# Kernel optimization log

Hardware: AMD Instinct MI355X
Metric: run time of the kernel (lower is better)

## Reference

```python
import jax, jax.numpy as jnp
import numpy as np

D_MODEL = 1024
N_HEADS = 16
D_K = D_MODEL // N_HEADS
ROPE_BASE = 10000.0


def _rope_cos_sin(seq_len, dim):
    # matches calc_rope_theta: freqs over even indices of head dim
    freqs = jnp.arange(0, dim, 2, dtype=jnp.float32) / dim
    inv_freq = 1.0 / (ROPE_BASE ** freqs)                      # [dim/2]
    pos = jnp.arange(seq_len, dtype=jnp.float32)               # [S]
    ang = pos[:, None] * inv_freq[None, :]                     # [S, dim/2]
    return jnp.cos(ang), jnp.sin(ang)


def _apply_rope(x, cos, sin):
    # x: [N, S, dk]; complex pairs are consecutive elements (view_as_complex)
    x0 = x[..., 0::2]
    x1 = x[..., 1::2]
    r = x0 * cos - x1 * sin
    i = x0 * sin + x1 * cos
    return jnp.stack([r, i], axis=-1).reshape(x.shape)


def setup_inputs() -> dict:
    key = jax.random.key(0)
    ks = jax.random.split(key, 11)
    B, S, D = 4, 1024, D_MODEL
    w = lambda k: jax.random.normal(k, (D, D), dtype=jnp.float32) * 0.02
    b = lambda k: jax.random.normal(k, (D,), dtype=jnp.float32) * 0.02
    return {
        "q": jax.random.normal(ks[0], (B, S, D), dtype=jnp.float32),
        "k": jax.random.normal(ks[1], (B, S, D), dtype=jnp.float32),
        "v": jax.random.normal(ks[2], (B, S, D), dtype=jnp.float32),
        "Wq": w(ks[3]), "bq": b(ks[4]),
        "Wk": w(ks[5]), "bk": b(ks[6]),
        "Wv": w(ks[7]), "bv": b(ks[8]),
        "Wo": w(ks[9]), "bo": b(ks[10]),
    }


def reference(q, k, v, Wq, bq, Wk, bk, Wv, bv, Wo, bo):
    B, S, D = q.shape
    H, dk = N_HEADS, D_K
    qp = (q @ Wq + bq).reshape(B, S, H, dk)
    kp = (k @ Wk + bk).reshape(B, S, H, dk)
    vp = (v @ Wv + bv).reshape(B, S, H, dk)

    cos, sin = _rope_cos_sin(S, dk)
    # Faithful to source: raw reshape (B,S,H,dk)->(-1,S,dk) before RoPE
    qp = _apply_rope(qp.reshape(-1, S, dk), cos, sin).reshape(B, S, H, dk)
    kp = _apply_rope(kp.reshape(-1, S, dk), cos, sin).reshape(B, S, H, dk)

    qh = qp.transpose(0, 2, 1, 3)  # [B,H,S,dk]
    kh = kp.transpose(0, 2, 1, 3)
    vh = vp.transpose(0, 2, 1, 3)

    scores = jnp.einsum("bhqd,bhkd->bhqk", qh, kh) / jnp.sqrt(jnp.float32(dk))
    attn = jax.nn.softmax(scores, axis=-1)
    out = jnp.einsum("bhqk,bhkd->bhqd", attn, vh)
    out = out.transpose(0, 2, 1, 3).reshape(B, S, D)
    return out @ Wo + bo
```

## Files before the change

### kernel.cpp

```cpp
#include <hip/hip_runtime.h>

typedef __attribute__((ext_vector_type(8))) short bf16x8;
typedef __attribute__((ext_vector_type(4))) short short4v;
typedef __attribute__((ext_vector_type(4))) float f32x4;
typedef __attribute__((ext_vector_type(2))) unsigned u32x2;

#define MFMA16x16x32(a, b, c) __builtin_amdgcn_mfma_f32_16x16x32_bf16((a), (b), (c), 0, 0, 0)

__device__ __forceinline__ short f2bf(float f) {
    unsigned u = __builtin_bit_cast(unsigned, f);
    u += 0x7FFFu + ((u >> 16) & 1u);
    return (short)(u >> 16);
}

__device__ __forceinline__ unsigned cvtpk(float lo, float hi) {
    unsigned r;
    asm("v_cvt_pk_bf16_f32 %0, %1, %2" : "=v"(r) : "v"(lo), "v"(hi));
    return r;
}

__device__ __forceinline__ void gl_lds16(const void* g, void* l) {
    __builtin_amdgcn_global_load_lds((__attribute__((address_space(1))) void*)g,
                                     (__attribute__((address_space(3))) void*)l,
                                     16, 0, 0);
}

__device__ __forceinline__ void cvt16(const float* __restrict__ p, bf16x8& lo, bf16x8& hi) {
    f32x4 a = *(const f32x4*)(p);
    f32x4 b = *(const f32x4*)(p + 4);
    f32x4 c = *(const f32x4*)(p + 8);
    f32x4 d = *(const f32x4*)(p + 12);
#pragma unroll
    for (int i = 0; i < 4; ++i) {
        lo[i]     = f2bf(a[i]);
        lo[i + 4] = f2bf(b[i]);
        hi[i]     = f2bf(c[i]);
        hi[i + 4] = f2bf(d[i]);
    }
}

__global__ __launch_bounds__(256) void prep(const float* __restrict__ q,
                                            const float* __restrict__ k,
                                            const float* __restrict__ v,
                                            const float* __restrict__ w0,
                                            const float* __restrict__ w1,
                                            const float* __restrict__ w2,
                                            const float* __restrict__ w3,
                                            short* __restrict__ y,
                                            short* __restrict__ wt) {
    __shared__ short t[64][80];
    int bid = blockIdx.x, tid = threadIdx.x;
    if (bid < 3072) {
        int sel = bid >> 10;
        const float* x = sel == 0 ? q : (sel == 1 ? k : v);
        short* yy = y + (size_t)sel * (1 << 22);
        int i = ((bid & 1023) * 256 + tid) * 16;
        bf16x8 lo, hi;
        cvt16(x + i, lo, hi);
        *(bf16x8*)(yy + i)     = lo;
        *(bf16x8*)(yy + i + 8) = hi;
        return;
    }
    int tz = bid - 3072;
    int z = tz >> 8, rem = tz & 255, bx = rem & 15, by = rem >> 4;
    const float* W = z == 0 ? w0 : (z == 1 ? w1 : (z == 2 ? w2 : w3));
    short* Wt = wt + (size_t)z * (1 << 20);
    int sr = tid >> 2, sc = (tid & 3) * 16;
    bf16x8 lo, hi;
    cvt16(W + (by * 64 + sr) * 1024 + bx * 64 + sc, lo, hi);
    *(bf16x8*)&t[sr][sc]     = lo;
    *(bf16x8*)&t[sr][sc + 8] = hi;
    __syncthreads();
    bf16x8 o0, o1;
#pragma unroll
    for (int i = 0; i < 8; ++i) {
        o0[i] = t[sc + i][sr];
        o1[i] = t[sc + 8 + i][sr];
    }
    short* dst = Wt + (bx * 64 + sr) * 1024 + by * 64 + sc;
    *(bf16x8*)(dst)     = o0;
    *(bf16x8*)(dst + 8) = o1;
}

__global__ __launch_bounds__(512) void gemm_qkv(const short* __restrict__ A0,
                                                const short* __restrict__ A1,
                                                const short* __restrict__ A2,
                                                const short* __restrict__ wt,
                                                const float* __restrict__ b0,
                                                const float* __restrict__ b1,
                                                const float* __restrict__ b2,
                                                short* __restrict__ d0,
                                                short* __restrict__ d1,
                                                short* __restrict__ d2,
                                                int zoff) {
    __shared__ short As[3][128 * 64];
    __shared__ short Bs[3][128 * 64];
    const int K = 1024;
    int flat = blockIdx.x;
    int xcd = flat & 7, j = flat >> 3;
    int bm = xcd * 4 + (j & 3);
    int bn = (j >> 2) & 7;
    int z  = zoff + (j >> 5);
    const short* A    = z == 0 ? A0 : (z == 1 ? A1 : A2);
    const short* Bt   = wt + (size_t)z * (1 << 20);
    const float* bias = z == 0 ? b0 : (z == 1 ? b1 : b2);
    short* dst        = z == 0 ? d0 : (z == 1 ? d1 : d2);

    int tid = threadIdx.x;
    int wave = tid >> 6, lane = tid & 63;
    int quad = lane >> 4, l16 = lane & 15;
    int wm = (wave >> 2) * 64, wn = (wave & 3) * 32;
    int swr = l16 & 7;

    f32x4 acc[4][2] = {};

    auto stage = [&](int b, int t) {
        int kb = t * 64;
#pragma unroll
        for (int jj = 0; jj < 2; ++jj) {
            int c = jj * 512 + tid;
            int row = c >> 3, sl = c & 7;
            gl_lds16(A + (bm * 128 + row) * K + kb + ((sl ^ (row & 7)) * 8),
                     &As[b][c * 8]);
        }
#pragma unroll
        for (int jj = 0; jj < 2; ++jj) {
            int c = jj * 512 + tid;
            int row = c >> 3, sl = c & 7;
            gl_lds16(Bt + (bn * 128 + row) * K + kb + ((sl ^ (row & 7)) * 8),
                     &Bs[b][c * 8]);
        }
    };

    stage(0, 0);
    stage(1, 1);

    int cur = 0;
    for (int t = 0; t < 16; ++t) {
        asm volatile("s_waitcnt vmcnt(4)" ::: "memory");
        __builtin_amdgcn_sched_barrier(0);
        __builtin_amdgcn_s_barrier();
        __builtin_amdgcn_sched_barrier(0);
        int pre = cur >= 1 ? cur - 1 : 2;
        stage(pre, (t + 2) & 15);
#pragma unroll
        for (int ks = 0; ks < 2; ++ks) {
            bf16x8 bf[2], af[4];
#pragma unroll
            for (int ni = 0; ni < 2; ++ni)
                bf[ni] = *(const bf16x8*)
                    &Bs[cur][(wn + ni * 16 + l16) * 64 + (((ks * 4 + quad) ^ swr) * 8)];
#pragma unroll
            for (int mi = 0; mi < 4; ++mi)
                af[mi] = *(const bf16x8*)
                    &As[cur][(wm + mi * 16 + l16) * 64 + (((ks * 4 + quad) ^ swr) * 8)];
            __builtin_amdgcn_s_setprio(1);
#pragma unroll
            for (int mi = 0; mi < 4; ++mi)
#pragma unroll
                for (int ni = 0; ni < 2; ++ni)
                    acc[mi][ni] = MFMA16x16x32(af[mi], bf[ni], acc[mi][ni]);
            __builtin_amdgcn_s_setprio(0);
        }
        cur = cur < 2 ? cur + 1 : 0;
    }

    int row0 = bm * 128 + wm;
    int col0 = bn * 128 + wn;
#pragma unroll
    for (int mi = 0; mi < 4; ++mi) {
#pragma unroll
        for (int ni = 0; ni < 2; ++ni) {
            int gn = col0 + ni * 16 + l16;
            float bv = bias[gn];
            f32x4 c = acc[mi][ni];
            int h = gn >> 6, dd = gn & 63;
            if (z < 2) {
                float inv = exp2f(-(float)(dd >> 1) * 0.41524101186092029f);
#pragma unroll
                for (int r = 0; r < 4; ++r) {
                    int gm = row0 + mi * 16 + quad * 4 + r;
                    int s = gm & 1023, b = gm >> 10;
                    int p = ((s << 4) + h) & 1023;
                    float val = c[r] + bv;
                    float partner = __shfl_xor(val, 1);
                    float sn, cs;
                    __sincosf((float)p * inv, &sn, &cs);
                    float res = (dd & 1) ? fmaf(partner, sn, val * cs)
                                         : fmaf(val, cs, -(partner * sn));
                    dst[((b * 16 + h) * 1024 + s) * 64 + dd] = f2bf(res);
                }
            } else {
                int gm0 = row0 + mi * 16 + quad * 4;
                int s0 = gm0 & 1023, b = gm0 >> 10;
                short4v pack;
#pragma unroll
                for (int r = 0; r < 4; ++r) pack[r] = f2bf(c[r] + bv);
                *(short4v*)&dst[((b * 16 + h) * 64 + dd) * 1024 + s0] = pack;
            }
        }
    }
}

__global__ __launch_bounds__(512) void gemm_o(const short* __restrict__ A,
                                              const short* __restrict__ Bt,
                                              const float* __restrict__ bias,
                                              float* __restrict__ dst) {
    __shared__ short As[3][128 * 64];
    __shared__ short Bs[3][128 * 64];
    const int K = 1024;
    int flat = blockIdx.x;
    int xcd = flat & 7, j = flat >> 3;
    int bm = xcd * 4 + (j & 3);
    int bn = (j >> 2) & 7;

    int tid = threadIdx.x;
    int wave = tid >> 6, lane = tid & 63;
    int quad = lane >> 4, l16 = lane & 15;
    int wm = (wave >> 2) * 64, wn = (wave & 3) * 32;
    int swr = l16 & 7;

    f32x4 acc[4][2] = {};

    auto stage = [&](int b, int t) {
        int kb = t * 64;
#pragma unroll
        for (int jj = 0; jj < 2; ++jj) {
            int c = jj * 512 + tid;
            int row = c >> 3, sl = c & 7;
            gl_lds16(A + (bm * 128 + row) * K + kb + ((sl ^ (row & 7)) * 8),
                     &As[b][c * 8]);
        }
#pragma unroll
        for (int jj = 0; jj < 2; ++jj) {
            int c = jj * 512 + tid;
            int row = c >> 3, sl = c & 7;
            gl_lds16(Bt + (bn * 128 + row) * K + kb + ((sl ^ (row & 7)) * 8),
                     &Bs[b][c * 8]);
        }
    };

    stage(0, 0);
    stage(1, 1);

    int cur = 0;
    for (int t = 0; t < 16; ++t) {
        asm volatile("s_waitcnt vmcnt(4)" ::: "memory");
        __builtin_amdgcn_sched_barrier(0);
        __builtin_amdgcn_s_barrier();
        __builtin_amdgcn_sched_barrier(0);
        int pre = cur >= 1 ? cur - 1 : 2;
        stage(pre, (t + 2) & 15);
#pragma unroll
        for (int ks = 0; ks < 2; ++ks) {
            bf16x8 bf[2], af[4];
#pragma unroll
            for (int ni = 0; ni < 2; ++ni)
                bf[ni] = *(const bf16x8*)
                    &Bs[cur][(wn + ni * 16 + l16) * 64 + (((ks * 4 + quad) ^ swr) * 8)];
#pragma unroll
            for (int mi = 0; mi < 4; ++mi)
                af[mi] = *(const bf16x8*)
                    &As[cur][(wm + mi * 16 + l16) * 64 + (((ks * 4 + quad) ^ swr) * 8)];
            __builtin_amdgcn_s_setprio(1);
#pragma unroll
            for (int mi = 0; mi < 4; ++mi)
#pragma unroll
                for (int ni = 0; ni < 2; ++ni)
                    acc[mi][ni] = MFMA16x16x32(af[mi], bf[ni], acc[mi][ni]);
            __builtin_amdgcn_s_setprio(0);
        }
        cur = cur < 2 ? cur + 1 : 0;
    }

    int row0 = bm * 128 + wm;
    int col0 = bn * 128 + wn;
#pragma unroll
    for (int mi = 0; mi < 4; ++mi) {
#pragma unroll
        for (int ni = 0; ni < 2; ++ni) {
            int gn = col0 + ni * 16 + l16;
            float bv = bias[gn];
            f32x4 c = acc[mi][ni];
#pragma unroll
            for (int r = 0; r < 4; ++r) {
                int gm = row0 + mi * 16 + quad * 4 + r;
                dst[gm * 1024 + gn] = c[r] + bv;
            }
        }
    }
}

__global__ __launch_bounds__(512) void attn_kernel(const short* __restrict__ Qh,
                                                   const short* __restrict__ Kh,
                                                   const short* __restrict__ Vt,
                                                   short* __restrict__ O) {
    __shared__ short Ks[3][32 * 64];
    __shared__ short Vs[3][64 * 32];
    __shared__ short Pl[8][16 * 40];
    int tid = threadIdx.x;
    int wave = tid >> 6, lane = tid & 63;
    int quad = lane >> 4, l16 = lane & 15;
    int bh = blockIdx.x & 63, qt = blockIdx.x >> 6;
    int qrow = qt * 128 + wave * 16;

    const short* Qp = Qh + (bh * 1024 + qrow) * 64;
    bf16x8 aq[2];
#pragma unroll
    for (int kh = 0; kh < 2; ++kh)
        aq[kh] = *(const bf16x8*)&Qp[l16 * 64 + kh * 32 + quad * 8];

    const short* Kp = Kh + bh * 1024 * 64;
    const short* Vp = Vt + bh * 64 * 1024;

    int ck = tid & 255;
    bool isV = tid >= 256;
    int krow = ck >> 3;
    int vrow = ck >> 2;
    int ksrc = krow * 64 + (((ck & 7) ^ (krow & 7)) * 8);
    int vsrc = vrow * 1024 + ((((ck & 3) ^ (vrow & 3) ^ ((vrow >> 2) & 3)) & 3) * 8);

    int ksw  = l16 & 7;
    int vswr = (l16 & 3) ^ ((l16 >> 2) & 3);

    float lsum = 0.f;
    f32x4 oa[4] = {};

    if (!isV) { gl_lds16(Kp + ksrc, &Ks[0][ck * 8]);
                gl_lds16(Kp + 32 * 64 + ksrc, &Ks[1][ck * 8]); }
    else      { gl_lds16(Vp + vsrc, &Vs[0][ck * 8]);
                gl_lds16(Vp + 32 + vsrc, &Vs[1][ck * 8]); }

    short* Pw = &Pl[wave][0];

    int cur = 0;
    for (int kb = 0; kb < 1024; kb += 32) {
        asm volatile("s_waitcnt vmcnt(1)" ::: "memory");
        __builtin_amdgcn_sched_barrier(0);
        __builtin_amdgcn_s_barrier();
        __builtin_amdgcn_sched_barrier(0);
        int pre = cur >= 1 ? cur - 1 : 2;
        int kb2 = (kb + 64) & 1023;
        if (!isV) gl_lds16(Kp + kb2 * 64 + ksrc, &Ks[pre][ck * 8]);
        else      gl_lds16(Vp + kb2 + vsrc,      &Vs[pre][ck * 8]);

#pragma unroll
        for (int g = 0; g < 2; ++g) {
            f32x4 s = {};
            __builtin_amdgcn_s_setprio(1);
#pragma unroll
            for (int kh = 0; kh < 2; ++kh) {
                bf16x8 ak = *(const bf16x8*)
                    &Ks[cur][(g * 16 + l16) * 64 + (((kh * 4 + quad) ^ ksw) * 8)];
                s = MFMA16x16x32(ak, aq[kh], s);
            }
            __builtin_amdgcn_s_setprio(0);
            float p[4];
#pragma unroll
            for (int r = 0; r < 4; ++r) {
                p[r] = exp2f(s[r] * 0.18033688011112042f);
                lsum += p[r];
            }
            u32x2 w;
            w[0] = cvtpk(p[0], p[1]);
            w[1] = cvtpk(p[2], p[3]);
            *(u32x2*)&Pw[l16 * 40 + g * 16 + quad * 4] = w;
        }

        bf16x8 bv[4];
#pragma unroll
        for (int t = 0; t < 4; ++t)
            bv[t] = *(const bf16x8*)&Vs[cur][(t * 16 + l16) * 32 + ((quad ^ vswr) * 8)];

        asm volatile("s_waitcnt lgkmcnt(0)" ::: "memory");
        bf16x8 ap = *(const bf16x8*)&Pw[l16 * 40 + quad * 8];

        __builtin_amdgcn_s_setprio(1);
#pragma unroll
        for (int t = 0; t < 4; ++t)
            oa[t] = MFMA16x16x32(ap, bv[t], oa[t]);
        __builtin_amdgcn_s_setprio(0);

        cur = cur < 2 ? cur + 1 : 0;
    }

    lsum += __shfl_xor(lsum, 16);
    lsum += __shfl_xor(lsum, 32);
    float inv[4];
#pragma unroll
    for (int r = 0; r < 4; ++r)
        inv[r] = 1.0f / __shfl(lsum, (lane & 48) + ((lane >> 4) & 3) * 4 + r);

    int b = bh >> 4, h = bh & 15;
#pragma unroll
    for (int t = 0; t < 4; ++t)
#pragma unroll
        for (int r = 0; r < 4; ++r) {
            int s = qrow + quad * 4 + r;
            O[(b * 1024 + s) * 1024 + h * 64 + t * 16 + l16] = f2bf(oa[t][r] * inv[r]);
        }
}

extern "C" void kernel_launch(void* const* d_in, const int* in_sizes, int n_in,
                              void* d_out, int out_size, void* d_ws, size_t ws_size,
                              hipStream_t stream) {
    const float* q  = (const float*)d_in[0];
    const float* k  = (const float*)d_in[1];
    const float* v  = (const float*)d_in[2];
    const float* Wq = (const float*)d_in[3];
    const float* bq = (const float*)d_in[4];
    const float* Wk = (const float*)d_in[5];
    const float* bk = (const float*)d_in[6];
    const float* Wv = (const float*)d_in[7];
    const float* bv = (const float*)d_in[8];
    const float* Wo = (const float*)d_in[9];
    const float* bo = (const float*)d_in[10];

    short* qb   = (short*)d_ws;
    short* kbuf = qb + (4 << 20);
    short* vb   = kbuf + (4 << 20);
    short* wt   = vb + (4 << 20);
    short* wto  = wt + (3 << 20);
    short* obuf = kbuf;

    short* qh  = (short*)d_out;
    short* kh  = qh + (4 << 20);
    float* out = (float*)d_out;

    bool batch3 = ws_size >= ((size_t)40 << 20);
    short* vt = batch3 ? qb + (16 << 20) : qb;

    prep<<<4096, 256, 0, stream>>>(q, k, v, Wq, Wk, Wv, Wo, qb, wt);

    if (batch3) {
        gemm_qkv<<<768, 512, 0, stream>>>(qb, kbuf, vb, wt, bq, bk, bv,
                                          qh, kh, vt, 0);
    } else {
        gemm_qkv<<<512, 512, 0, stream>>>(qb, kbuf, vb, wt, bq, bk, bv,
                                          qh, kh, vt, 0);
        gemm_qkv<<<256, 512, 0, stream>>>(qb, kbuf, vb, wt, bq, bk, bv,
                                          qh, kh, vt, 2);
    }

    attn_kernel<<<512, 512, 0, stream>>>(qh, kh, vt, obuf);

    gemm_o<<<256, 512, 0, stream>>>(obuf, wto, bo, out);
}
```

Before: 211.2 us.

## Enlarge QKV GEMM tiles to 256x256 with double-buffered LDS pipeline

```diff
diff --git a/kernel.cpp b/kernel.cpp
--- a/kernel.cpp
+++ b/kernel.cpp
@@ -93,14 +93,15 @@
                                                 short* __restrict__ d1,
                                                 short* __restrict__ d2,
                                                 int zoff) {
-    __shared__ short As[3][128 * 64];
-    __shared__ short Bs[3][128 * 64];
+    __shared__ short As[2][256 * 64];
+    __shared__ short Bs[2][256 * 64];
     const int K = 1024;
     int flat = blockIdx.x;
     int xcd = flat & 7, j = flat >> 3;
-    int bm = xcd * 4 + (j & 3);
-    int bn = (j >> 2) & 7;
-    int z  = zoff + (j >> 5);
+    int z  = zoff + (j >> 3);
+    int r  = j & 7;
+    int bm = xcd * 2 + (r >> 2);
+    int bn = r & 3;
     const short* A    = z == 0 ? A0 : (z == 1 ? A1 : A2);
     const short* Bt   = wt + (size_t)z * (1 << 20);
     const float* bias = z == 0 ? b0 : (z == 1 ? b1 : b2);
@@ -109,68 +110,72 @@
     int tid = threadIdx.x;
     int wave = tid >> 6, lane = tid & 63;
     int quad = lane >> 4, l16 = lane & 15;
-    int wm = (wave >> 2) * 64, wn = (wave & 3) * 32;
+    int wr = (wave >> 2) * 128, wc = (wave & 3) * 64;
     int swr = l16 & 7;
 
-    f32x4 acc[4][2] = {};
+    f32x4 acc[8][4] = {};
 
     auto stage = [&](int b, int t) {
         int kb = t * 64;
 #pragma unroll
-        for (int jj = 0; jj < 2; ++jj) {
+        for (int jj = 0; jj < 4; ++jj) {
             int c = jj * 512 + tid;
             int row = c >> 3, sl = c & 7;
-            gl_lds16(A + (bm * 128 + row) * K + kb + ((sl ^ (row & 7)) * 8),
+            gl_lds16(A + (bm * 256 + row) * K + kb + ((sl ^ (row & 7)) * 8),
                      &As[b][c * 8]);
         }
 #pragma unroll
-        for (int jj = 0; jj < 2; ++jj) {
+        for (int jj = 0; jj < 4; ++jj) {
             int c = jj * 512 + tid;
             int row = c >> 3, sl = c & 7;
-            gl_lds16(Bt + (bn * 128 + row) * K + kb + ((sl ^ (row & 7)) * 8),
+            gl_lds16(Bt + (bn * 256 + row) * K + kb + ((sl ^ (row & 7)) * 8),
                      &Bs[b][c * 8]);
         }
     };
 
     stage(0, 0);
-    stage(1, 1);
-
-    int cur = 0;
+
     for (int t = 0; t < 16; ++t) {
-        asm volatile("s_waitcnt vmcnt(4)" ::: "memory");
+        int cur = t & 1;
+        if (t < 15) {
+            stage(cur ^ 1, t + 1);
+            asm volatile("s_waitcnt vmcnt(8)" ::: "memory");
+        } else {
+            asm volatile("s_waitcnt vmcnt(0)" ::: "memory");
+        }
         __builtin_amdgcn_sched_barrier(0);
         __builtin_amdgcn_s_barrier();
         __builtin_amdgcn_sched_barrier(0);
-        int pre = cur >= 1 ? cur - 1 : 2;
-        stage(pre, (t + 2) & 15);
 #pragma unroll
         for (int ks = 0; ks < 2; ++ks) {
-            bf16x8 bf[2], af[4];
-#pragma unroll
-            for (int ni = 0; ni < 2; ++ni)
+            bf16x8 bf[4], af[8];
+#pragma unroll
+            for (int ni = 0; ni < 4; ++ni)
                 bf[ni] = *(const bf16x8*)
-                    &Bs[cur][(wn + ni * 16 + l16) * 64 + (((ks * 4 + quad) ^ swr) * 8)];
-#pragma unroll
-            for (int mi = 0; mi < 4; ++mi)
+                    &Bs[cur][(wc + ni * 16 + l16) * 64 + (((ks * 4 + quad) ^ swr) * 8)];
+#pragma unroll
+            for (int mi = 0; mi < 8; ++mi)
                 af[mi] = *(const bf16x8*)
-                    &As[cur][(wm + mi * 16 + l16) * 64 + (((ks * 4 + quad) ^ swr) * 8)];
+                    &As[cur][(wr + mi * 16 + l16) * 64 + (((ks * 4 + quad) ^ swr) * 8)];
             __builtin_amdgcn_s_setprio(1);
 #pragma unroll
-            for (int mi = 0; mi < 4; ++mi)
-#pragma unroll
-                for (int ni = 0; ni < 2; ++ni)
+            for (int mi = 0; mi < 8; ++mi)
+#pragma unroll
+                for (int ni = 0; ni < 4; ++ni)
                     acc[mi][ni] = MFMA16x16x32(af[mi], bf[ni], acc[mi][ni]);
             __builtin_amdgcn_s_setprio(0);
         }
-        cur = cur < 2 ? cur + 1 : 0;
-    }
-
-    int row0 = bm * 128 + wm;
-    int col0 = bn * 128 + wn;
-#pragma unroll
-    for (int mi = 0; mi < 4; ++mi) {
-#pragma unroll
-        for (int ni = 0; ni < 2; ++ni) {
+        __builtin_amdgcn_sched_barrier(0);
+        __builtin_amdgcn_s_barrier();
+        __builtin_amdgcn_sched_barrier(0);
+    }
+
+    int row0 = bm * 256 + wr;
+    int col0 = bn * 256 + wc;
+#pragma unroll
+    for (int mi = 0; mi < 8; ++mi) {
+#pragma unroll
+        for (int ni = 0; ni < 4; ++ni) {
             int gn = col0 + ni * 16 + l16;
             float bv = bias[gn];
             f32x4 c = acc[mi][ni];
@@ -178,11 +183,11 @@
             if (z < 2) {
                 float inv = exp2f(-(float)(dd >> 1) * 0.41524101186092029f);
 #pragma unroll
-                for (int r = 0; r < 4; ++r) {
-                    int gm = row0 + mi * 16 + quad * 4 + r;
+                for (int rr = 0; rr < 4; ++rr) {
+                    int gm = row0 + mi * 16 + quad * 4 + rr;
                     int s = gm & 1023, b = gm >> 10;
                     int p = ((s << 4) + h) & 1023;
-                    float val = c[r] + bv;
+                    float val = c[rr] + bv;
                     float partner = __shfl_xor(val, 1);
                     float sn, cs;
                     __sincosf((float)p * inv, &sn, &cs);
@@ -195,7 +200,7 @@
                 int s0 = gm0 & 1023, b = gm0 >> 10;
                 short4v pack;
 #pragma unroll
-                for (int r = 0; r < 4; ++r) pack[r] = f2bf(c[r] + bv);
+                for (int rr = 0; rr < 4; ++rr) pack[rr] = f2bf(c[rr] + bv);
                 *(short4v*)&dst[((b * 16 + h) * 64 + dd) * 1024 + s0] = pack;
             }
         }
@@ -433,13 +438,13 @@
     prep<<<4096, 256, 0, stream>>>(q, k, v, Wq, Wk, Wv, Wo, qb, wt);
 
     if (batch3) {
-        gemm_qkv<<<768, 512, 0, stream>>>(qb, kbuf, vb, wt, bq, bk, bv,
+        gemm_qkv<<<192, 512, 0, stream>>>(qb, kbuf, vb, wt, bq, bk, bv,
                                           qh, kh, vt, 0);
     } else {
-        gemm_qkv<<<512, 512, 0, stream>>>(qb, kbuf, vb, wt, bq, bk, bv,
+        gemm_qkv<<<128, 512, 0, stream>>>(qb, kbuf, vb, wt, bq, bk, bv,
                                           qh, kh, vt, 0);
-        gemm_qkv<<<256, 512, 0, stream>>>(qb, kbuf, vb, wt, bq, bk, bv,
-                                          qh, kh, vt, 2);
+        gemm_qkv<<<64, 512, 0, stream>>>(qb, kbuf, vb, wt, bq, bk, bv,
+                                         qh, kh, vt, 2);
     }
 
     attn_kernel<<<512, 512, 0, stream>>>(qh, kh, vt, obuf);
```

Result: no change. 213.0 us (+0.9%).

## Double attention key-block size to 64 with unified K/V LDS loading

Applied to the files above, without the earlier changes.

```diff
diff --git a/kernel.cpp b/kernel.cpp
--- a/kernel.cpp
+++ b/kernel.cpp
@@ -295,9 +295,9 @@
                                                    const short* __restrict__ Kh,
                                                    const short* __restrict__ Vt,
                                                    short* __restrict__ O) {
-    __shared__ short Ks[3][32 * 64];
-    __shared__ short Vs[3][64 * 32];
-    __shared__ short Pl[8][16 * 40];
+    __shared__ short Ks[3][64 * 64];
+    __shared__ short Vs[3][64 * 64];
+    __shared__ short Pl[8][16 * 72];
     int tid = threadIdx.x;
     int wave = tid >> 6, lane = tid & 63;
     int quad = lane >> 4, l16 = lane & 15;
@@ -313,45 +313,41 @@
     const short* Kp = Kh + bh * 1024 * 64;
     const short* Vp = Vt + bh * 64 * 1024;
 
-    int ck = tid & 255;
-    bool isV = tid >= 256;
-    int krow = ck >> 3;
-    int vrow = ck >> 2;
-    int ksrc = krow * 64 + (((ck & 7) ^ (krow & 7)) * 8);
-    int vsrc = vrow * 1024 + ((((ck & 3) ^ (vrow & 3) ^ ((vrow >> 2) & 3)) & 3) * 8);
-
-    int ksw  = l16 & 7;
-    int vswr = (l16 & 3) ^ ((l16 >> 2) & 3);
+    int srow = tid >> 3, ssl = tid & 7;
+    int ssw  = (ssl ^ (srow & 7)) * 8;
+    int ksrc = srow * 64 + ssw;
+    int vsrc = srow * 1024 + ssw;
+    int rsw  = l16 & 7;
 
     float lsum = 0.f;
     f32x4 oa[4] = {};
 
-    if (!isV) { gl_lds16(Kp + ksrc, &Ks[0][ck * 8]);
-                gl_lds16(Kp + 32 * 64 + ksrc, &Ks[1][ck * 8]); }
-    else      { gl_lds16(Vp + vsrc, &Vs[0][ck * 8]);
-                gl_lds16(Vp + 32 + vsrc, &Vs[1][ck * 8]); }
+    gl_lds16(Kp + ksrc,            &Ks[0][tid * 8]);
+    gl_lds16(Vp + vsrc,            &Vs[0][tid * 8]);
+    gl_lds16(Kp + 64 * 64 + ksrc,  &Ks[1][tid * 8]);
+    gl_lds16(Vp + 64 + vsrc,       &Vs[1][tid * 8]);
 
     short* Pw = &Pl[wave][0];
 
     int cur = 0;
-    for (int kb = 0; kb < 1024; kb += 32) {
-        asm volatile("s_waitcnt vmcnt(1)" ::: "memory");
+    for (int kb = 0; kb < 1024; kb += 64) {
+        asm volatile("s_waitcnt vmcnt(2)" ::: "memory");
         __builtin_amdgcn_sched_barrier(0);
         __builtin_amdgcn_s_barrier();
         __builtin_amdgcn_sched_barrier(0);
         int pre = cur >= 1 ? cur - 1 : 2;
-        int kb2 = (kb + 64) & 1023;
-        if (!isV) gl_lds16(Kp + kb2 * 64 + ksrc, &Ks[pre][ck * 8]);
-        else      gl_lds16(Vp + kb2 + vsrc,      &Vs[pre][ck * 8]);
-
-#pragma unroll
-        for (int g = 0; g < 2; ++g) {
+        int kb2 = (kb + 128) & 1023;
+        gl_lds16(Kp + kb2 * 64 + ksrc, &Ks[pre][tid * 8]);
+        gl_lds16(Vp + kb2 + vsrc,      &Vs[pre][tid * 8]);
+
+#pragma unroll
+        for (int g = 0; g < 4; ++g) {
             f32x4 s = {};
             __builtin_amdgcn_s_setprio(1);
 #pragma unroll
             for (int kh = 0; kh < 2; ++kh) {
                 bf16x8 ak = *(const bf16x8*)
-                    &Ks[cur][(g * 16 + l16) * 64 + (((kh * 4 + quad) ^ ksw) * 8)];
+                    &Ks[cur][(g * 16 + l16) * 64 + (((kh * 4 + quad) ^ rsw) * 8)];
                 s = MFMA16x16x32(ak, aq[kh], s);
             }
             __builtin_amdgcn_s_setprio(0);
@@ -364,25 +360,31 @@
             u32x2 w;
             w[0] = cvtpk(p[0], p[1]);
             w[1] = cvtpk(p[2], p[3]);
-            *(u32x2*)&Pw[l16 * 40 + g * 16 + quad * 4] = w;
-        }
-
-        bf16x8 bv[4];
-#pragma unroll
-        for (int t = 0; t < 4; ++t)
-            bv[t] = *(const bf16x8*)&Vs[cur][(t * 16 + l16) * 32 + ((quad ^ vswr) * 8)];
+            *(u32x2*)&Pw[l16 * 72 + g * 16 + quad * 4] = w;
+        }
+
+        bf16x8 bv0[4], bv1[4];
+#pragma unroll
+        for (int t = 0; t < 4; ++t) {
+            bv0[t] = *(const bf16x8*)&Vs[cur][(t * 16 + l16) * 64 + ((quad ^ rsw) * 8)];
+            bv1[t] = *(const bf16x8*)&Vs[cur][(t * 16 + l16) * 64 + (((4 + quad) ^ rsw) * 8)];
+        }
 
         asm volatile("s_waitcnt lgkmcnt(0)" ::: "memory");
-        bf16x8 ap = *(const bf16x8*)&Pw[l16 * 40 + quad * 8];
+        bf16x8 ap0 = *(const bf16x8*)&Pw[l16 * 72 + quad * 8];
+        bf16x8 ap1 = *(const bf16x8*)&Pw[l16 * 72 + 32 + quad * 8];
 
         __builtin_amdgcn_s_setprio(1);
 #pragma unroll
-        for (int t = 0; t < 4; ++t)
-            oa[t] = MFMA16x16x32(ap, bv[t], oa[t]);
+        for (int t = 0; t < 4; ++t) {
+            oa[t] = MFMA16x16x32(ap0, bv0[t], oa[t]);
+            oa[t] = MFMA16x16x32(ap1, bv1[t], oa[t]);
+        }
         __builtin_amdgcn_s_setprio(0);
 
         cur = cur < 2 ? cur + 1 : 0;
     }
+    asm volatile("s_waitcnt vmcnt(0)" ::: "memory");
 
     lsum += __shfl_xor(lsum, 16);
     lsum += __shfl_xor(lsum, 32);
```

After: 208.9 us. Within noise of the previous version (-1.1%).
